# Kernel optimization log

Measured on AMD Instinct MI355X. Metric: run time of the kernel, lower is better.

## Reference

```python
import jax, jax.numpy as jnp
import numpy as np

B, C, F, H = 8, 256, 128, 256  # batch, channels(nodes), bn_features, hidden_size


def setup_inputs() -> dict:
    key = jax.random.key(0)
    k1, k2, k3, k4 = jax.random.split(key, 4)
    s1 = 1.0 / np.sqrt(2 * F)  # torch Linear default init scale
    s2 = 1.0 / np.sqrt(H)
    return {
        "xa": jax.random.normal(k1, (B, C, F), dtype=jnp.float32),
        "W1": jax.random.uniform(k2, (H, 2 * F), jnp.float32, -s1, s1),
        "b1": jax.random.uniform(k3, (H,), jnp.float32, -s1, s1),
        "w2": jax.random.uniform(k4, (H,), jnp.float32, -s2, s2),
        "b2": jnp.zeros((), jnp.float32),
    }


def reference(xa, W1, b1, w2, b2):
    # Linear over cat([x_i, x_j]) == x_i @ Wa^T + x_j @ Wb^T  (split first layer;
    # identical math to torch's concat+Linear, avoids the (B,C,C,2F) concat).
    f = xa.shape[-1]
    Wa, Wb = W1[:, :f], W1[:, f:]
    a = jnp.einsum('bif,hf->bih', xa, Wa)          # (B,C,H)
    c = jnp.einsum('bjf,hf->bjh', xa, Wb)          # (B,C,H)
    h = jax.nn.relu(a[:, :, None, :] + c[:, None, :, :] + b1)  # (B,C,C,H)
    edge_logits = jnp.einsum('bijh,h->bij', h, w2) + b2         # (B,C,C)
    return jax.nn.sigmoid(edge_logits)
```

## Files before the change

### kernel.cpp

```cpp
#include <hip/hip_runtime.h>


typedef _Float16 h2 __attribute__((ext_vector_type(2)));
typedef _Float16 h8 __attribute__((ext_vector_type(8)));
typedef float    f4 __attribute__((ext_vector_type(4)));

constexpr int B  = 8;
constexpr int C  = 256;
constexpr int F  = 128;
constexpr int H  = 256;
constexpr int F2 = 2 * F;
constexpr int HOCT = H / 8;

#if __has_builtin(__builtin_amdgcn_fdot2)
__device__ __forceinline__ float fdot2(h2 a, h2 b, float c) {
    return __builtin_amdgcn_fdot2(a, b, c, false);
}
#else
__device__ __forceinline__ float fdot2(h2 a, h2 b, float c) {
    return c + (float)a.x * (float)b.x + (float)a.y * (float)b.y;
}
#endif

union HU { h8 v; h2 p[4]; };

__device__ __forceinline__ h2 pkrtz(float x, float y) {
    return __builtin_bit_cast(h2, __builtin_amdgcn_cvt_pkrtz(x, y));
}

__device__ __forceinline__ h8 cvt8(float4 a, float4 b) {
    HU u;
    u.p[0] = pkrtz(a.x, a.y);
    u.p[1] = pkrtz(a.z, a.w);
    u.p[2] = pkrtz(b.x, b.y);
    u.p[3] = pkrtz(b.z, b.w);
    return u.v;
}

__global__ __launch_bounds__(256) void k1_mfma(
    const float* __restrict__ xa, const float* __restrict__ W1,
    const float* __restrict__ b1, const float* __restrict__ w2,
    _Float16* __restrict__ Ah, _Float16* __restrict__ CP8,
    _Float16* __restrict__ w2h)
{
    const int t  = threadIdx.x;
    const int w  = blockIdx.x * 4 + (t >> 6);
    const int l  = t & 63;
    const int mg = w >> 4;
    const int h0 = (w & 15) * 16;
    const int lm = l & 15;
    const int lk = (l >> 4) * 8;
    const int m0 = mg * 32;

    h8 af[2][4];
    const float* xp0 = xa + (size_t)(m0 + lm) * F + lk;
    const float* xp1 = xp0 + 16 * F;
    #pragma unroll
    for (int kk = 0; kk < 4; ++kk) {
        af[0][kk] = cvt8(*(const float4*)(xp0 + kk * 32),
                         *(const float4*)(xp0 + kk * 32 + 4));
        af[1][kk] = cvt8(*(const float4*)(xp1 + kk * 32),
                         *(const float4*)(xp1 + kk * 32 + 4));
    }

    const float* wp = W1 + (size_t)(h0 + lm) * F2 + lk;
    f4 accA0 = {0.f,0.f,0.f,0.f}, accA1 = {0.f,0.f,0.f,0.f};
    f4 accC0 = {0.f,0.f,0.f,0.f}, accC1 = {0.f,0.f,0.f,0.f};
    #pragma unroll
    for (int kk = 0; kk < 4; ++kk) {
        h8 ba = cvt8(*(const float4*)(wp + kk * 32),
                     *(const float4*)(wp + kk * 32 + 4));
        h8 bb = cvt8(*(const float4*)(wp + F + kk * 32),
                     *(const float4*)(wp + F + kk * 32 + 4));
        accA0 = __builtin_amdgcn_mfma_f32_16x16x32_f16(af[0][kk], ba, accA0, 0, 0, 0);
        accC0 = __builtin_amdgcn_mfma_f32_16x16x32_f16(af[0][kk], bb, accC0, 0, 0, 0);
        accA1 = __builtin_amdgcn_mfma_f32_16x16x32_f16(af[1][kk], ba, accA1, 0, 0, 0);
        accC1 = __builtin_amdgcn_mfma_f32_16x16x32_f16(af[1][kk], bb, accC1, 0, 0, 0);
    }

    const int h  = h0 + lm;
    const float bh = b1[h];
    #pragma unroll
    for (int mt = 0; mt < 2; ++mt) {
        const f4 aA = mt ? accA1 : accA0;
        const f4 aC = mt ? accC1 : accC0;
        const int mb = m0 + mt * 16 + (l >> 4) * 4;
        #pragma unroll
        for (int r = 0; r < 4; ++r) {
            const int m = mb + r;
            Ah[(size_t)m * H + h] = (_Float16)(aA[r] + bh);
            CP8[(((size_t)((m >> 8) * HOCT + (h >> 3)) * C + (m & 255)) << 3) + (h & 7)]
                = (_Float16)aC[r];
        }
    }

    if (blockIdx.x == 0 && t < 128) {
        float2 wv = ((const float2*)w2)[t];
        h2 hv = {(_Float16)wv.x, (_Float16)wv.y};
        ((h2*)w2h)[t] = hv;
    }
}

constexpr int TI = 8;
constexpr int HS = 4;
constexpr int JW = 128;

__global__ __launch_bounds__(512) void k2_pair(
    const _Float16* __restrict__ Ah, const _Float16* __restrict__ CP8,
    const _Float16* __restrict__ w2h, const float* __restrict__ b2p,
    float* __restrict__ out)
{
    __shared__ float red[(HS - 1) * TI * JW];
    const int t   = threadIdx.x;
    const int jl  = t & (JW - 1);
    const int hs  = t >> 7;
    const int blk = blockIdx.x;
    const int jh  = blk & 1;
    const int it  = (blk >> 1) & 31;
    const int b   = blk >> 6;
    const int i0  = it * TI;
    const int j   = jh * JW + jl;

    float acc[TI];
    #pragma unroll
    for (int ii = 0; ii < TI; ++ii) acc[ii] = 0.f;

    const int g0 = hs * (HOCT / HS);
    const _Float16* Ab = Ah + (size_t)(b * C + i0) * H;

    #pragma unroll 2
    for (int g = 0; g < HOCT / HS; ++g) {
        const int hb = g0 + g;
        h8 cc = *(const h8*)(CP8 + (((size_t)(b * HOCT + hb) * C + j) << 3));
        HU uw; uw.v = *(const h8*)(w2h + hb * 8);
        #pragma unroll
        for (int ii = 0; ii < TI; ++ii) {
            h8 ao = *(const h8*)(Ab + ii * H + hb * 8);
            const h8 z = {0, 0, 0, 0, 0, 0, 0, 0};
            h8 s = __builtin_elementwise_max(ao + cc, z);
            HU us; us.v = s;
            float a0 = acc[ii];
            a0 = fdot2(us.p[0], uw.p[0], a0);
            a0 = fdot2(us.p[1], uw.p[1], a0);
            a0 = fdot2(us.p[2], uw.p[2], a0);
            a0 = fdot2(us.p[3], uw.p[3], a0);
            acc[ii] = a0;
        }
    }

    if (hs > 0) {
        #pragma unroll
        for (int ii = 0; ii < TI; ++ii)
            red[((hs - 1) * TI + ii) * JW + jl] = acc[ii];
    }
    __syncthreads();
    if (hs == 0) {
        const float bb = b2p[0];
        #pragma unroll
        for (int ii = 0; ii < TI; ++ii) {
            float x = acc[ii]
                    + red[(0 * TI + ii) * JW + jl]
                    + red[(1 * TI + ii) * JW + jl]
                    + red[(2 * TI + ii) * JW + jl] + bb;
            out[(size_t)(b * C + i0 + ii) * C + j] = 1.f / (1.f + __expf(-x));
        }
    }
}

extern "C" void kernel_launch(void* const* d_in, const int* in_sizes, int n_in,
                              void* d_out, int out_size, void* d_ws, size_t ws_size,
                              hipStream_t stream) {
    const float* xa = (const float*)d_in[0];
    const float* W1 = (const float*)d_in[1];
    const float* b1 = (const float*)d_in[2];
    const float* w2 = (const float*)d_in[3];
    const float* b2 = (const float*)d_in[4];
    float* out = (float*)d_out;

    _Float16* Ah  = (_Float16*)d_ws;
    _Float16* CP8 = Ah  + (size_t)B * C * H;
    _Float16* w2h = CP8 + (size_t)B * H * C;

    k1_mfma<<<256, 256, 0, stream>>>(xa, W1, b1, w2, Ah, CP8, w2h);
    k2_pair<<<512, 512, 0, stream>>>(Ah, CP8, w2h, b2, out);
}
```

Measured before the change: 23.55 us.

## Transpose MFMA operands for vectorized fp16 stores and double grid sizes

The projection kernel now gives each wave one 16-row tile and swaps the MFMA operand order, so each lane holds four consecutive hidden values. That lets it write Ah and CP8 with packed 4-wide fp16 stores instead of scattered scalar stores. The launch grid doubles to 512 blocks. The pair kernel halves its i-tile to 4 rows and doubles its grid to 1024 blocks for more parallelism, at the cost of less reuse of each loaded CP8 vector and more redundant weight loads.

```diff
diff --git a/kernel.cpp b/kernel.cpp
--- a/kernel.cpp
+++ b/kernel.cpp
@@ -2,6 +2,7 @@
 
 
 typedef _Float16 h2 __attribute__((ext_vector_type(2)));
+typedef _Float16 h4 __attribute__((ext_vector_type(4)));
 typedef _Float16 h8 __attribute__((ext_vector_type(8)));
 typedef float    f4 __attribute__((ext_vector_type(4)));
 
@@ -37,6 +38,10 @@
     return u.v;
 }
 
+__device__ __forceinline__ float4 ldg4(const float* p) {
+    return *(const float4*)p;
+}
+
 __global__ __launch_bounds__(256) void k1_mfma(
     const float* __restrict__ xa, const float* __restrict__ W1,
     const float* __restrict__ b1, const float* __restrict__ w2,
@@ -46,62 +51,51 @@
     const int t  = threadIdx.x;
     const int w  = blockIdx.x * 4 + (t >> 6);
     const int l  = t & 63;
-    const int mg = w >> 4;
+    const int mt = w >> 4;
     const int h0 = (w & 15) * 16;
     const int lm = l & 15;
     const int lk = (l >> 4) * 8;
-    const int m0 = mg * 32;
+    const int lq = (l >> 4) * 4;
+    const int m0 = mt * 16;
 
-    h8 af[2][4];
-    const float* xp0 = xa + (size_t)(m0 + lm) * F + lk;
-    const float* xp1 = xp0 + 16 * F;
+    const float* xp = xa + (size_t)(m0 + lm) * F + lk;
+    const float* wp = W1 + (size_t)(h0 + lm) * F2 + lk;
+
+    f4 accA = {0.f, 0.f, 0.f, 0.f};
+    f4 accC = {0.f, 0.f, 0.f, 0.f};
     #pragma unroll
     for (int kk = 0; kk < 4; ++kk) {
-        af[0][kk] = cvt8(*(const float4*)(xp0 + kk * 32),
-                         *(const float4*)(xp0 + kk * 32 + 4));
-        af[1][kk] = cvt8(*(const float4*)(xp1 + kk * 32),
-                         *(const float4*)(xp1 + kk * 32 + 4));
+        h8 xf = cvt8(ldg4(xp + kk * 32), ldg4(xp + kk * 32 + 4));
+        h8 wa = cvt8(ldg4(wp + kk * 32), ldg4(wp + kk * 32 + 4));
+        h8 wb = cvt8(ldg4(wp + F + kk * 32), ldg4(wp + F + kk * 32 + 4));
+        accA = __builtin_amdgcn_mfma_f32_16x16x32_f16(wa, xf, accA, 0, 0, 0);
+        accC = __builtin_amdgcn_mfma_f32_16x16x32_f16(wb, xf, accC, 0, 0, 0);
     }
 
-    const float* wp = W1 + (size_t)(h0 + lm) * F2 + lk;
-    f4 accA0 = {0.f,0.f,0.f,0.f}, accA1 = {0.f,0.f,0.f,0.f};
-    f4 accC0 = {0.f,0.f,0.f,0.f}, accC1 = {0.f,0.f,0.f,0.f};
-    #pragma unroll
-    for (int kk = 0; kk < 4; ++kk) {
-        h8 ba = cvt8(*(const float4*)(wp + kk * 32),
-                     *(const float4*)(wp + kk * 32 + 4));
-        h8 bb = cvt8(*(const float4*)(wp + F + kk * 32),
-                     *(const float4*)(wp + F + kk * 32 + 4));
-        accA0 = __builtin_amdgcn_mfma_f32_16x16x32_f16(af[0][kk], ba, accA0, 0, 0, 0);
-        accC0 = __builtin_amdgcn_mfma_f32_16x16x32_f16(af[0][kk], bb, accC0, 0, 0, 0);
-        accA1 = __builtin_amdgcn_mfma_f32_16x16x32_f16(af[1][kk], ba, accA1, 0, 0, 0);
-        accC1 = __builtin_amdgcn_mfma_f32_16x16x32_f16(af[1][kk], bb, accC1, 0, 0, 0);
+    const int m  = m0 + lm;
+    const int hq = h0 + lq;
+    {
+        const float4 bq = ldg4(b1 + hq);
+        h2 v01 = pkrtz(accA[0] + bq.x, accA[1] + bq.y);
+        h2 v23 = pkrtz(accA[2] + bq.z, accA[3] + bq.w);
+        h4 v; v[0] = v01[0]; v[1] = v01[1]; v[2] = v23[0]; v[3] = v23[1];
+        *(h4*)(Ah + (size_t)m * H + hq) = v;
     }
-
-    const int h  = h0 + lm;
-    const float bh = b1[h];
-    #pragma unroll
-    for (int mt = 0; mt < 2; ++mt) {
-        const f4 aA = mt ? accA1 : accA0;
-        const f4 aC = mt ? accC1 : accC0;
-        const int mb = m0 + mt * 16 + (l >> 4) * 4;
-        #pragma unroll
-        for (int r = 0; r < 4; ++r) {
-            const int m = mb + r;
-            Ah[(size_t)m * H + h] = (_Float16)(aA[r] + bh);
-            CP8[(((size_t)((m >> 8) * HOCT + (h >> 3)) * C + (m & 255)) << 3) + (h & 7)]
-                = (_Float16)aC[r];
-        }
+    {
+        h2 v01 = pkrtz(accC[0], accC[1]);
+        h2 v23 = pkrtz(accC[2], accC[3]);
+        h4 v; v[0] = v01[0]; v[1] = v01[1]; v[2] = v23[0]; v[3] = v23[1];
+        *(h4*)(CP8 + (((size_t)((m >> 8) * HOCT + (hq >> 3)) * C + (m & 255)) << 3)
+                   + (hq & 7)) = v;
     }
 
     if (blockIdx.x == 0 && t < 128) {
         float2 wv = ((const float2*)w2)[t];
-        h2 hv = {(_Float16)wv.x, (_Float16)wv.y};
-        ((h2*)w2h)[t] = hv;
+        ((h2*)w2h)[t] = pkrtz(wv.x, wv.y);
     }
 }
 
-constexpr int TI = 8;
+constexpr int TI = 4;
 constexpr int HS = 4;
 constexpr int JW = 128;
 
@@ -116,8 +110,8 @@
     const int hs  = t >> 7;
     const int blk = blockIdx.x;
     const int jh  = blk & 1;
-    const int it  = (blk >> 1) & 31;
-    const int b   = blk >> 6;
+    const int it  = (blk >> 1) & 63;
+    const int b   = blk >> 7;
     const int i0  = it * TI;
     const int j   = jh * JW + jl;
 
@@ -181,6 +175,6 @@
     _Float16* CP8 = Ah  + (size_t)B * C * H;
     _Float16* w2h = CP8 + (size_t)B * H * C;
 
-    k1_mfma<<<256, 256, 0, stream>>>(xa, W1, b1, w2, Ah, CP8, w2h);
-    k2_pair<<<512, 512, 0, stream>>>(Ah, CP8, w2h, b2, out);
+    k1_mfma<<<512, 256, 0, stream>>>(xa, W1, b1, w2, Ah, CP8, w2h);
+    k2_pair<<<1024, 512, 0, stream>>>(Ah, CP8, w2h, b2, out);
 }
```

After: 26.47 us. 12.4% more time.
